# Performance work log

Measured on AMD Instinct MI355X. Metric: run time of the kernel, lower is better.

Reference implementation:

```python
import jax, jax.numpy as jnp
import numpy as np

D_MODEL = 1024
NHEAD = 16
D_HEAD = D_MODEL // NHEAD


def setup_inputs() -> dict:
    key = jax.random.key(0)
    ks = jax.random.split(key, 9)
    B, S = 2, 2048
    scale = 1.0 / np.sqrt(D_MODEL)
    x = jax.random.normal(ks[0], (B, S, D_MODEL), dtype=jnp.float32)
    Wq = jax.random.normal(ks[1], (D_MODEL, D_MODEL), dtype=jnp.float32) * scale
    Wk = jax.random.normal(ks[2], (D_MODEL, D_MODEL), dtype=jnp.float32) * scale
    Wv = jax.random.normal(ks[3], (D_MODEL, D_MODEL), dtype=jnp.float32) * scale
    Wo = jax.random.normal(ks[4], (D_MODEL, D_MODEL), dtype=jnp.float32) * scale
    bq = jax.random.normal(ks[5], (D_MODEL,), dtype=jnp.float32) * 0.01
    bk = jax.random.normal(ks[6], (D_MODEL,), dtype=jnp.float32) * 0.01
    bv = jax.random.normal(ks[7], (D_MODEL,), dtype=jnp.float32) * 0.01
    bo = jax.random.normal(ks[8], (D_MODEL,), dtype=jnp.float32) * 0.01
    return {"x": x, "Wq": Wq, "bq": bq, "Wk": Wk, "bk": bk,
            "Wv": Wv, "bv": bv, "Wo": Wo, "bo": bo}


def reference(x, Wq, bq, Wk, bk, Wv, bv, Wo, bo):
    B, S, D = x.shape
    H, Dh = NHEAD, D_HEAD
    # projections; weights stored as (in, out) so y = x @ W + b
    def split_heads(t):  # [B,S,D] -> [B,H,S,Dh]
        return t.reshape(B, S, H, Dh).transpose(0, 2, 1, 3)
    q = split_heads(x @ Wq + bq)
    k = split_heads(x @ Wk + bk)
    v = split_heads(x @ Wv + bv)
    scale = 1.0 / jnp.sqrt(jnp.asarray(Dh, dtype=x.dtype))
    attn = jnp.einsum("bhqd,bhkd->bhqk", q, k) * scale  # [B,H,S,S]
    attn = jax.nn.softmax(attn, axis=-1)
    out = jnp.einsum("bhqk,bhkd->bhqd", attn, v)  # [B,H,S,Dh]
    out = out.transpose(0, 2, 1, 3).reshape(B, S, D)
    return out @ Wo + bo
```

## Files before the change

kernel.cpp:

```cpp
#include <hip/hip_runtime.h>
#include <hip/hip_bf16.h>
#include <stdint.h>
#include <stddef.h>

typedef __bf16 b16;
typedef __bf16 b16x4 __attribute__((ext_vector_type(4)));
typedef __bf16 b16x8 __attribute__((ext_vector_type(8)));
typedef float  f32x4 __attribute__((ext_vector_type(4)));

#define LOG2E 1.4426950408889634f
#define QSCALE (0.125f * LOG2E)

#if __has_builtin(__builtin_amdgcn_exp2f)
#define EXP2F(x) __builtin_amdgcn_exp2f(x)
#else
#define EXP2F(x) exp2f(x)
#endif

typedef __attribute__((address_space(1))) void gvoid;
typedef __attribute__((address_space(3))) void svoid;

__device__ __forceinline__ void async_cp16(void* lds, const void* g) {
    __builtin_amdgcn_global_load_lds((gvoid*)(void*)g, (svoid*)lds, 16, 0, 0);
}

#define SW(r) ((((r) & 7)) ^ (((r) >> 1) & 4))

__global__ __launch_bounds__(256) void k_cvt_x(const float* __restrict__ x,
                                               b16* __restrict__ xb) {
    int i = (blockIdx.x * 256 + threadIdx.x) * 4;
    float4 v = *(const float4*)(x + i);
    b16x4 o = { (b16)v.x, (b16)v.y, (b16)v.z, (b16)v.w };
    *(b16x4*)(xb + i) = o;
}

__global__ __launch_bounds__(256) void k_transpose(const float* __restrict__ Wq,
                                                   const float* __restrict__ Wk,
                                                   const float* __restrict__ Wv,
                                                   const float* __restrict__ Wo,
                                                   b16* __restrict__ WtQKV,
                                                   b16* __restrict__ Wot) {
    __shared__ float t[32][33];
    const int z = blockIdx.z;
    const float* W = (z == 0) ? Wq : (z == 1) ? Wk : (z == 2) ? Wv : Wo;
    const int k0 = blockIdx.x * 32, n0 = blockIdx.y * 32;
    const int tr = threadIdx.x >> 3, tc4 = (threadIdx.x & 7) * 4;
    float4 v = *(const float4*)(W + (size_t)(k0 + tr) * 1024 + n0 + tc4);
    t[tr][tc4 + 0] = v.x; t[tr][tc4 + 1] = v.y;
    t[tr][tc4 + 2] = v.z; t[tr][tc4 + 3] = v.w;
    __syncthreads();
    b16* dst = (z < 3) ? (WtQKV + ((size_t)z << 20)) : Wot;
    b16x4 o = { (b16)t[tc4 + 0][tr], (b16)t[tc4 + 1][tr],
                (b16)t[tc4 + 2][tr], (b16)t[tc4 + 3][tr] };
    *(b16x4*)(dst + (size_t)(n0 + tr) * 1024 + k0 + tc4) = o;
}

__device__ __forceinline__ void gemm128_core(const b16* __restrict__ Ab,
                                             const b16* __restrict__ Bb,
                                             b16* As, b16* Bs, int tid,
                                             f32x4 acc[4][4]) {
    const int lane = tid & 63, wave = tid >> 6;
    const int wm = wave & 1, wn = wave >> 1;
    const int quad = lane >> 4, lc = lane & 15;
    const int ci0 = tid, ci1 = tid + 256;
    for (int k0 = 0; k0 < 1024; k0 += 32) {
        __syncthreads();
        async_cp16(As + ci0 * 8, Ab + (ci0 >> 2) * 1024 + k0 + (ci0 & 3) * 8);
        async_cp16(As + ci1 * 8, Ab + (ci1 >> 2) * 1024 + k0 + (ci1 & 3) * 8);
        async_cp16(Bs + ci0 * 8, Bb + (ci0 >> 2) * 1024 + k0 + (ci0 & 3) * 8);
        async_cp16(Bs + ci1 * 8, Bb + (ci1 >> 2) * 1024 + k0 + (ci1 & 3) * 8);
        __syncthreads();
        b16x8 af[4], bfr[4];
#pragma unroll
        for (int mt = 0; mt < 4; ++mt)
            af[mt] = *(const b16x8*)(As + (wm * 64 + mt * 16 + lc) * 32 + quad * 8);
#pragma unroll
        for (int nt = 0; nt < 4; ++nt)
            bfr[nt] = *(const b16x8*)(Bs + (wn * 64 + nt * 16 + lc) * 32 + quad * 8);
#pragma unroll
        for (int mt = 0; mt < 4; ++mt)
#pragma unroll
            for (int nt = 0; nt < 4; ++nt)
                acc[mt][nt] = __builtin_amdgcn_mfma_f32_16x16x32_bf16(
                    af[mt], bfr[nt], acc[mt][nt], 0, 0, 0);
    }
}

__global__ __launch_bounds__(256, 2) void k_gemm_qkv(
    const b16* __restrict__ A, const b16* __restrict__ Bt,
    const float* __restrict__ bq, const float* __restrict__ bk,
    const float* __restrict__ bv,
    b16* __restrict__ Qg, b16* __restrict__ Kg, b16* __restrict__ Vtg) {
    __shared__ __align__(16) b16 As[128 * 32];
    __shared__ __align__(16) b16 Bs[128 * 32];
    const int bm = blockIdx.x, bn = blockIdx.y;
    const int tid = threadIdx.x;
    const int lane = tid & 63, wave = tid >> 6;
    const int wm = wave & 1, wn = wave >> 1;
    const int quad = lane >> 4, lc = lane & 15;

    f32x4 acc[4][4] = {};
    gemm128_core(A + (size_t)(bm * 128) * 1024, Bt + (size_t)(bn * 128) * 1024,
                 As, Bs, tid, acc);

    const int mat = bn >> 3;
    const float* bp = (mat == 0) ? bq : (mat == 1) ? bk : bv;
#pragma unroll
    for (int nt = 0; nt < 4; ++nt) {
        const int n = bn * 128 + wn * 64 + nt * 16 + lc;
        const int cm = n & 1023;
        const int h = cm >> 6, dh = cm & 63;
        const float bval = bp[cm];
#pragma unroll
        for (int mt = 0; mt < 4; ++mt) {
            const int m0 = bm * 128 + wm * 64 + mt * 16 + quad * 4;
            const int b = m0 >> 11;
            const int bh = b * 16 + h;
            const int s0 = m0 & 2047;
            if (mat == 2) {
                b16x4 o;
#pragma unroll
                for (int r = 0; r < 4; ++r) o[r] = (b16)(acc[mt][nt][r] + bval);
                *(b16x4*)(Vtg + (size_t)(bh * 64 + dh) * 2048 + s0) = o;
            } else if (mat == 0) {
#pragma unroll
                for (int r = 0; r < 4; ++r)
                    Qg[(size_t)(bh * 2048 + s0 + r) * 64 + dh] =
                        (b16)((acc[mt][nt][r] + bval) * QSCALE);
            } else {
#pragma unroll
                for (int r = 0; r < 4; ++r)
                    Kg[(size_t)(bh * 2048 + s0 + r) * 64 + dh] =
                        (b16)(acc[mt][nt][r] + bval);
            }
        }
    }
}

__device__ __forceinline__ void flash_stage(b16* Kd, b16* Vd,
                                            const b16* __restrict__ Kbh,
                                            const b16* __restrict__ Vbh,
                                            int kt, int tid) {
#pragma unroll
    for (int i = 0; i < 2; ++i) {
        const int ci = tid + i * 256;
        const int r = ci >> 3, cs = ci & 7;
        const int gc = cs ^ SW(r);
        async_cp16(Kd + ci * 8, Kbh + (size_t)(kt * 64 + r) * 64 + gc * 8);
        async_cp16(Vd + ci * 8, Vbh + (size_t)r * 2048 + kt * 64 + gc * 8);
    }
}

__global__ __launch_bounds__(256, 4) void k_flash(
    const b16* __restrict__ Qg, const b16* __restrict__ Kg,
    const b16* __restrict__ Vtg,
    float* __restrict__ Opart, float* __restrict__ lpart,
    b16* __restrict__ AO, int ktiles, int direct, int np) {
    __shared__ __align__(16) b16 Ks[2 * 64 * 64];
    __shared__ __align__(16) b16 Vs[2 * 64 * 64];
    __shared__ float Lred[4][32];

    const int bid = blockIdx.x;
    const int gstride = np << 5;
    const int qb = bid / gstride;
    const int rem = bid - qb * gstride;
    const int bh = rem / np;
    const int part = rem - bh * np;

    const int tid = threadIdx.x, lane = tid & 63, wave = tid >> 6;
    const int quad = lane >> 4, lc = lane & 15;

    const b16* Kbh = Kg + (size_t)bh * 2048 * 64;
    const b16* Vbh = Vtg + (size_t)bh * 64 * 2048;
    const int kt0 = part * ktiles, ktE = kt0 + ktiles;

    flash_stage(Ks, Vs, Kbh, Vbh, kt0, tid);

    const b16* Qbase = Qg + ((size_t)bh * 2048 + qb * 128 + wave * 32) * 64;
    b16x8 qf[2][2];
#pragma unroll
    for (int qt = 0; qt < 2; ++qt)
#pragma unroll
        for (int ch = 0; ch < 2; ++ch)
            qf[qt][ch] = *(const b16x8*)(Qbase + (qt * 16 + lc) * 64 + ch * 32 + quad * 8);

    f32x4 oacc[2][4] = {};
    float lsum[2] = {0.f, 0.f};

    for (int kt = kt0; kt < ktE; ++kt) {
        const int cur = (kt - kt0) & 1;
        const b16* Kc = Ks + cur * 4096;
        const b16* Vc = Vs + cur * 4096;

        if (kt + 1 < ktE) {
            flash_stage(Ks + (cur ^ 1) * 4096, Vs + (cur ^ 1) * 4096,
                        Kbh, Vbh, kt + 1, tid);
            asm volatile("s_waitcnt vmcnt(4)" ::: "memory");
        } else {
            asm volatile("s_waitcnt vmcnt(0)" ::: "memory");
        }
        __builtin_amdgcn_s_barrier();
        __builtin_amdgcn_sched_barrier(0);

#pragma unroll
        for (int ks = 0; ks < 2; ++ks) {
            b16x8 pf[2];
#pragma unroll
            for (int t = 0; t < 2; ++t) {
                const int krow = ks * 32 + (lc >> 2) * 8 + t * 4 + (lc & 3);
                b16x8 kf[2];
#pragma unroll
                for (int ch = 0; ch < 2; ++ch) {
                    const int slot = (ch * 4 + quad) ^ SW(krow);
                    kf[ch] = *(const b16x8*)(Kc + krow * 64 + slot * 8);
                }
#pragma unroll
                for (int qt = 0; qt < 2; ++qt) {
                    f32x4 s = {};
                    __builtin_amdgcn_s_setprio(1);
                    s = __builtin_amdgcn_mfma_f32_16x16x32_bf16(kf[0], qf[qt][0], s, 0, 0, 0);
                    s = __builtin_amdgcn_mfma_f32_16x16x32_bf16(kf[1], qf[qt][1], s, 0, 0, 0);
                    __builtin_amdgcn_s_setprio(0);
                    float e0 = EXP2F(s[0]), e1 = EXP2F(s[1]);
                    float e2 = EXP2F(s[2]), e3 = EXP2F(s[3]);
                    lsum[qt] += (e0 + e1) + (e2 + e3);
                    pf[qt][t * 4 + 0] = (b16)e0;
                    pf[qt][t * 4 + 1] = (b16)e1;
                    pf[qt][t * 4 + 2] = (b16)e2;
                    pf[qt][t * 4 + 3] = (b16)e3;
                }
            }
            b16x8 vf[4];
#pragma unroll
            for (int dt = 0; dt < 4; ++dt) {
                const int row = dt * 16 + lc;
                const int slot = (ks * 4 + quad) ^ SW(row);
                vf[dt] = *(const b16x8*)(Vc + row * 64 + slot * 8);
            }
            __builtin_amdgcn_s_setprio(1);
#pragma unroll
            for (int qt = 0; qt < 2; ++qt)
#pragma unroll
                for (int dt = 0; dt < 4; ++dt)
                    oacc[qt][dt] = __builtin_amdgcn_mfma_f32_16x16x32_bf16(
                        pf[qt], vf[dt], oacc[qt][dt], 0, 0, 0);
            __builtin_amdgcn_s_setprio(0);
        }

        __builtin_amdgcn_sched_barrier(0);
        __builtin_amdgcn_s_barrier();
    }

#pragma unroll
    for (int qt = 0; qt < 2; ++qt) {
        lsum[qt] += __shfl_xor(lsum[qt], 16, 64);
        lsum[qt] += __shfl_xor(lsum[qt], 32, 64);
    }

    if (!direct) {
        float* Op = Opart + ((size_t)(part * 32 + bh) * 2048 + qb * 128 + wave * 32) * 64;
#pragma unroll
        for (int qt = 0; qt < 2; ++qt)
#pragma unroll
            for (int dt = 0; dt < 4; ++dt)
#pragma unroll
                for (int r = 0; r < 4; ++r)
                    Op[(qt * 16 + quad * 4 + r) * 64 + dt * 16 + lc] = oacc[qt][dt][r];
        if (quad == 0) {
            float* lp = lpart + (size_t)(part * 32 + bh) * 2048 + qb * 128 + wave * 32;
#pragma unroll
            for (int qt = 0; qt < 2; ++qt) lp[qt * 16 + lc] = lsum[qt];
        }
    } else {
        if (quad == 0) {
#pragma unroll
            for (int qt = 0; qt < 2; ++qt) Lred[wave][qt * 16 + lc] = lsum[qt];
        }
        const int b = bh >> 4, h = bh & 15;
#pragma unroll
        for (int qt = 0; qt < 2; ++qt)
#pragma unroll
            for (int r = 0; r < 4; ++r) {
                const float inv = 1.0f / Lred[wave][qt * 16 + quad * 4 + r];
                const int s = qb * 128 + wave * 32 + qt * 16 + quad * 4 + r;
#pragma unroll
                for (int dt = 0; dt < 4; ++dt)
                    AO[(size_t)(b * 2048 + s) * 1024 + h * 64 + dt * 16 + lc] =
                        (b16)(oacc[qt][dt][r] * inv);
            }
    }
}

__global__ __launch_bounds__(256) void k_merge(const float* __restrict__ Opart,
                                               const float* __restrict__ lpart,
                                               b16* __restrict__ AO, int np) {
    const int bh = blockIdx.y;
    const int q = blockIdx.x * 16 + (threadIdx.x >> 4);
    const int d4 = (threadIdx.x & 15) * 4;
    const size_t qi = (size_t)bh * 2048 + q;
    f32x4 o = *(const f32x4*)(Opart + qi * 64 + d4);
    float l = lpart[qi];
    if (np == 2) {
        o += *(const f32x4*)(Opart + (qi + (size_t)32 * 2048) * 64 + d4);
        l += lpart[qi + (size_t)32 * 2048];
    }
    const float inv = 1.0f / l;
    const int b = bh >> 4, h = bh & 15;
    b16x4 ob = { (b16)(o[0] * inv), (b16)(o[1] * inv),
                 (b16)(o[2] * inv), (b16)(o[3] * inv) };
    *(b16x4*)(AO + (size_t)(b * 2048 + q) * 1024 + h * 64 + d4) = ob;
}

__global__ __launch_bounds__(256, 2) void k_gemm_out(
    const b16* __restrict__ A, const b16* __restrict__ Bt,
    const float* __restrict__ bo, float* __restrict__ out) {
    __shared__ __align__(16) b16 As[128 * 32];
    __shared__ __align__(16) b16 Bs[128 * 32];
    const int bm = blockIdx.x, bn = blockIdx.y;
    const int tid = threadIdx.x;
    const int lane = tid & 63, wave = tid >> 6;
    const int wm = wave & 1, wn = wave >> 1;
    const int quad = lane >> 4, lc = lane & 15;

    f32x4 acc[4][4] = {};
    gemm128_core(A + (size_t)(bm * 128) * 1024, Bt + (size_t)(bn * 128) * 1024,
                 As, Bs, tid, acc);

#pragma unroll
    for (int nt = 0; nt < 4; ++nt) {
        const int n = bn * 128 + wn * 64 + nt * 16 + lc;
        const float bval = bo[n];
#pragma unroll
        for (int mt = 0; mt < 4; ++mt) {
            const int m0 = bm * 128 + wm * 64 + mt * 16 + quad * 4;
#pragma unroll
            for (int r = 0; r < 4; ++r)
                out[(size_t)(m0 + r) * 1024 + n] = acc[mt][nt][r] + bval;
        }
    }
}

extern "C" void kernel_launch(void* const* d_in, const int* in_sizes, int n_in,
                              void* d_out, int out_size, void* d_ws, size_t ws_size,
                              hipStream_t stream) {
    const float* x  = (const float*)d_in[0];
    const float* Wq = (const float*)d_in[1];
    const float* bq = (const float*)d_in[2];
    const float* Wk = (const float*)d_in[3];
    const float* bk = (const float*)d_in[4];
    const float* Wv = (const float*)d_in[5];
    const float* bv = (const float*)d_in[6];
    const float* Wo = (const float*)d_in[7];
    const float* bo = (const float*)d_in[8];
    float* out = (float*)d_out;

    char* ws = (char*)d_ws;
    const size_t MB = 1024 * 1024;
    b16* Xb  = (b16*)(ws);
    b16* AO  = (b16*)(ws);
    b16* WtQ = (b16*)(ws + 8 * MB);
    b16* Wot = (b16*)(ws + 14 * MB);
    b16* Qg  = (b16*)(ws + 16 * MB);
    b16* Kg  = (b16*)(ws + 24 * MB);
    b16* Vtg = (b16*)(ws + 32 * MB);

    const size_t need2 = 40 * MB + 2 * (16 * MB) + 2 * 256 * 1024;
    const int np = (ws_size >= need2) ? 2 : 1;
    float* Opart = (float*)(ws + 40 * MB);
    float* lpart = (float*)(ws + 40 * MB + (size_t)np * 16 * MB);
    const int direct = (np == 1);

    k_cvt_x<<<4096, 256, 0, stream>>>(x, Xb);
    k_transpose<<<dim3(32, 32, 4), 256, 0, stream>>>(Wq, Wk, Wv, Wo, WtQ, Wot);
    k_gemm_qkv<<<dim3(32, 24), 256, 0, stream>>>(Xb, WtQ, bq, bk, bv, Qg, Kg, Vtg);
    k_flash<<<dim3(16 * 32 * np), 256, 0, stream>>>(Qg, Kg, Vtg, Opart, lpart, AO,
                                                    32 / np, direct, np);
    if (!direct)
        k_merge<<<dim3(128, 32), 256, 0, stream>>>(Opart, lpart, AO, np);
    k_gemm_out<<<dim3(32, 8), 256, 0, stream>>>(AO, Wot, bo, out);
}
```

Measured before the change: 197.1 us.

## Double-buffer GEMM loads, drop flash key split, fuse prep kernels

```diff
diff --git a/kernel.cpp b/kernel.cpp
--- a/kernel.cpp
+++ b/kernel.cpp
@@ -26,22 +26,29 @@
 
 #define SW(r) ((((r) & 7)) ^ (((r) >> 1) & 4))
 
-__global__ __launch_bounds__(256) void k_cvt_x(const float* __restrict__ x,
-                                               b16* __restrict__ xb) {
-    int i = (blockIdx.x * 256 + threadIdx.x) * 4;
-    float4 v = *(const float4*)(x + i);
-    b16x4 o = { (b16)v.x, (b16)v.y, (b16)v.z, (b16)v.w };
-    *(b16x4*)(xb + i) = o;
-}
-
-__global__ __launch_bounds__(256) void k_transpose(const float* __restrict__ Wq,
-                                                   const float* __restrict__ Wk,
-                                                   const float* __restrict__ Wv,
-                                                   const float* __restrict__ Wo,
-                                                   b16* __restrict__ WtQKV,
-                                                   b16* __restrict__ Wot) {
+__global__ __launch_bounds__(256) void k_prep(const float* __restrict__ x,
+                                              const float* __restrict__ Wq,
+                                              const float* __restrict__ Wk,
+                                              const float* __restrict__ Wv,
+                                              const float* __restrict__ Wo,
+                                              b16* __restrict__ Xb,
+                                              b16* __restrict__ WtQKV,
+                                              b16* __restrict__ Wot) {
+    const int z = blockIdx.z;
+    if (z == 4) {
+        const int blk = blockIdx.y * 32 + blockIdx.x;
+        const float* src = x + (size_t)blk * 4096;
+        b16* dst = Xb + (size_t)blk * 4096;
+#pragma unroll
+        for (int c = 0; c < 4; ++c) {
+            const int i = c * 1024 + threadIdx.x * 4;
+            float4 v = *(const float4*)(src + i);
+            b16x4 o = { (b16)v.x, (b16)v.y, (b16)v.z, (b16)v.w };
+            *(b16x4*)(dst + i) = o;
+        }
+        return;
+    }
     __shared__ float t[32][33];
-    const int z = blockIdx.z;
     const float* W = (z == 0) ? Wq : (z == 1) ? Wk : (z == 2) ? Wv : Wo;
     const int k0 = blockIdx.x * 32, n0 = blockIdx.y * 32;
     const int tr = threadIdx.x >> 3, tc4 = (threadIdx.x & 7) * 4;
@@ -55,35 +62,66 @@
     *(b16x4*)(dst + (size_t)(n0 + tr) * 1024 + k0 + tc4) = o;
 }
 
-__device__ __forceinline__ void gemm128_core(const b16* __restrict__ Ab,
-                                             const b16* __restrict__ Bb,
+__device__ __forceinline__ void gemm128_core(const b16* __restrict__ Ag,
+                                             const b16* __restrict__ Bg,
                                              b16* As, b16* Bs, int tid,
                                              f32x4 acc[4][4]) {
     const int lane = tid & 63, wave = tid >> 6;
     const int wm = wave & 1, wn = wave >> 1;
     const int quad = lane >> 4, lc = lane & 15;
     const int ci0 = tid, ci1 = tid + 256;
-    for (int k0 = 0; k0 < 1024; k0 += 32) {
-        __syncthreads();
-        async_cp16(As + ci0 * 8, Ab + (ci0 >> 2) * 1024 + k0 + (ci0 & 3) * 8);
-        async_cp16(As + ci1 * 8, Ab + (ci1 >> 2) * 1024 + k0 + (ci1 & 3) * 8);
-        async_cp16(Bs + ci0 * 8, Bb + (ci0 >> 2) * 1024 + k0 + (ci0 & 3) * 8);
-        async_cp16(Bs + ci1 * 8, Bb + (ci1 >> 2) * 1024 + k0 + (ci1 & 3) * 8);
-        __syncthreads();
+    const b16* a0 = Ag + (ci0 >> 2) * 1024 + (ci0 & 3) * 8;
+    const b16* a1 = Ag + (ci1 >> 2) * 1024 + (ci1 & 3) * 8;
+    const b16* b0 = Bg + (ci0 >> 2) * 1024 + (ci0 & 3) * 8;
+    const b16* b1 = Bg + (ci1 >> 2) * 1024 + (ci1 & 3) * 8;
+
+#define GSTAGE(BUF, K0) do {                                   \
+        async_cp16(As + (BUF) * 4096 + ci0 * 8, a0 + (K0));    \
+        async_cp16(As + (BUF) * 4096 + ci1 * 8, a1 + (K0));    \
+        async_cp16(Bs + (BUF) * 4096 + ci0 * 8, b0 + (K0));    \
+        async_cp16(Bs + (BUF) * 4096 + ci1 * 8, b1 + (K0));    \
+    } while (0)
+
+    auto gcompute = [&](int buf) {
+        const b16* Al = As + buf * 4096;
+        const b16* Bl = Bs + buf * 4096;
         b16x8 af[4], bfr[4];
 #pragma unroll
         for (int mt = 0; mt < 4; ++mt)
-            af[mt] = *(const b16x8*)(As + (wm * 64 + mt * 16 + lc) * 32 + quad * 8);
+            af[mt] = *(const b16x8*)(Al + (wm * 64 + mt * 16 + lc) * 32 + quad * 8);
 #pragma unroll
         for (int nt = 0; nt < 4; ++nt)
-            bfr[nt] = *(const b16x8*)(Bs + (wn * 64 + nt * 16 + lc) * 32 + quad * 8);
+            bfr[nt] = *(const b16x8*)(Bl + (wn * 64 + nt * 16 + lc) * 32 + quad * 8);
 #pragma unroll
         for (int mt = 0; mt < 4; ++mt)
 #pragma unroll
             for (int nt = 0; nt < 4; ++nt)
                 acc[mt][nt] = __builtin_amdgcn_mfma_f32_16x16x32_bf16(
                     af[mt], bfr[nt], acc[mt][nt], 0, 0, 0);
-    }
+    };
+
+    GSTAGE(0, 0);
+    for (int k0 = 0; k0 < 1024; k0 += 64) {
+        GSTAGE(1, k0 + 32);
+        asm volatile("s_waitcnt vmcnt(4)" ::: "memory");
+        __builtin_amdgcn_s_barrier();
+        __builtin_amdgcn_sched_barrier(0);
+        gcompute(0);
+        __builtin_amdgcn_sched_barrier(0);
+        __builtin_amdgcn_s_barrier();
+        if (k0 + 64 < 1024) {
+            GSTAGE(0, k0 + 64);
+            asm volatile("s_waitcnt vmcnt(4)" ::: "memory");
+        } else {
+            asm volatile("s_waitcnt vmcnt(0)" ::: "memory");
+        }
+        __builtin_amdgcn_s_barrier();
+        __builtin_amdgcn_sched_barrier(0);
+        gcompute(1);
+        __builtin_amdgcn_sched_barrier(0);
+        __builtin_amdgcn_s_barrier();
+    }
+#undef GSTAGE
 }
 
 __global__ __launch_bounds__(256, 2) void k_gemm_qkv(
@@ -91,8 +129,8 @@
     const float* __restrict__ bq, const float* __restrict__ bk,
     const float* __restrict__ bv,
     b16* __restrict__ Qg, b16* __restrict__ Kg, b16* __restrict__ Vtg) {
-    __shared__ __align__(16) b16 As[128 * 32];
-    __shared__ __align__(16) b16 Bs[128 * 32];
+    __shared__ __align__(16) b16 As[2 * 128 * 32];
+    __shared__ __align__(16) b16 Bs[2 * 128 * 32];
     const int bm = blockIdx.x, bn = blockIdx.y;
     const int tid = threadIdx.x;
     const int lane = tid & 63, wave = tid >> 6;
@@ -137,185 +175,128 @@
     }
 }
 
-__device__ __forceinline__ void flash_stage(b16* Kd, b16* Vd,
-                                            const b16* __restrict__ Kbh,
-                                            const b16* __restrict__ Vbh,
-                                            int kt, int tid) {
-#pragma unroll
-    for (int i = 0; i < 2; ++i) {
-        const int ci = tid + i * 256;
-        const int r = ci >> 3, cs = ci & 7;
-        const int gc = cs ^ SW(r);
-        async_cp16(Kd + ci * 8, Kbh + (size_t)(kt * 64 + r) * 64 + gc * 8);
-        async_cp16(Vd + ci * 8, Vbh + (size_t)r * 2048 + kt * 64 + gc * 8);
-    }
-}
-
 __global__ __launch_bounds__(256, 4) void k_flash(
     const b16* __restrict__ Qg, const b16* __restrict__ Kg,
-    const b16* __restrict__ Vtg,
-    float* __restrict__ Opart, float* __restrict__ lpart,
-    b16* __restrict__ AO, int ktiles, int direct, int np) {
+    const b16* __restrict__ Vtg, b16* __restrict__ AO) {
     __shared__ __align__(16) b16 Ks[2 * 64 * 64];
     __shared__ __align__(16) b16 Vs[2 * 64 * 64];
-    __shared__ float Lred[4][32];
+    __shared__ float Lred[4][16];
 
     const int bid = blockIdx.x;
-    const int gstride = np << 5;
-    const int qb = bid / gstride;
-    const int rem = bid - qb * gstride;
-    const int bh = rem / np;
-    const int part = rem - bh * np;
+    const int qb = bid >> 5;
+    const int bh = bid & 31;
 
     const int tid = threadIdx.x, lane = tid & 63, wave = tid >> 6;
     const int quad = lane >> 4, lc = lane & 15;
 
     const b16* Kbh = Kg + (size_t)bh * 2048 * 64;
     const b16* Vbh = Vtg + (size_t)bh * 64 * 2048;
-    const int kt0 = part * ktiles, ktE = kt0 + ktiles;
-
-    flash_stage(Ks, Vs, Kbh, Vbh, kt0, tid);
-
-    const b16* Qbase = Qg + ((size_t)bh * 2048 + qb * 128 + wave * 32) * 64;
-    b16x8 qf[2][2];
-#pragma unroll
-    for (int qt = 0; qt < 2; ++qt)
-#pragma unroll
-        for (int ch = 0; ch < 2; ++ch)
-            qf[qt][ch] = *(const b16x8*)(Qbase + (qt * 16 + lc) * 64 + ch * 32 + quad * 8);
-
-    f32x4 oacc[2][4] = {};
-    float lsum[2] = {0.f, 0.f};
-
-    for (int kt = kt0; kt < ktE; ++kt) {
-        const int cur = (kt - kt0) & 1;
-        const b16* Kc = Ks + cur * 4096;
-        const b16* Vc = Vs + cur * 4096;
-
-        if (kt + 1 < ktE) {
-            flash_stage(Ks + (cur ^ 1) * 4096, Vs + (cur ^ 1) * 4096,
-                        Kbh, Vbh, kt + 1, tid);
+
+    const int ci0 = tid, ci1 = tid + 256;
+    const int r0 = ci0 >> 3, gc0 = (ci0 & 7) ^ SW(r0);
+    const int r1 = ci1 >> 3, gc1 = (ci1 & 7) ^ SW(r1);
+    const b16* pK0 = Kbh + r0 * 64 + gc0 * 8;
+    const b16* pK1 = Kbh + r1 * 64 + gc1 * 8;
+    const b16* pV0 = Vbh + (size_t)r0 * 2048 + gc0 * 8;
+    const b16* pV1 = Vbh + (size_t)r1 * 2048 + gc1 * 8;
+
+#define FSTAGE(BUF) do {                                   \
+        async_cp16(Ks + (BUF) * 4096 + ci0 * 8, pK0);      \
+        async_cp16(Ks + (BUF) * 4096 + ci1 * 8, pK1);      \
+        async_cp16(Vs + (BUF) * 4096 + ci0 * 8, pV0);      \
+        async_cp16(Vs + (BUF) * 4096 + ci1 * 8, pV1);      \
+        pK0 += 4096; pK1 += 4096; pV0 += 64; pV1 += 64;    \
+    } while (0)
+
+    FSTAGE(0);
+
+    const b16* Qbase = Qg + ((size_t)bh * 2048 + qb * 64 + wave * 16) * 64;
+    b16x8 qf0 = *(const b16x8*)(Qbase + lc * 64 + quad * 8);
+    b16x8 qf1 = *(const b16x8*)(Qbase + lc * 64 + 32 + quad * 8);
+
+    f32x4 oacc[4] = {};
+    float lsum = 0.f;
+
+    auto flash_tile = [&](const b16* Kc, const b16* Vc) {
+#pragma unroll
+        for (int ks = 0; ks < 2; ++ks) {
+            b16x8 pf;
+#pragma unroll
+            for (int t = 0; t < 2; ++t) {
+                const int krow = ks * 32 + (lc >> 2) * 8 + t * 4 + (lc & 3);
+                b16x8 kf0 = *(const b16x8*)(Kc + krow * 64 + ((0 * 4 + quad) ^ SW(krow)) * 8);
+                b16x8 kf1 = *(const b16x8*)(Kc + krow * 64 + ((1 * 4 + quad) ^ SW(krow)) * 8);
+                f32x4 s = {};
+                __builtin_amdgcn_s_setprio(1);
+                s = __builtin_amdgcn_mfma_f32_16x16x32_bf16(kf0, qf0, s, 0, 0, 0);
+                s = __builtin_amdgcn_mfma_f32_16x16x32_bf16(kf1, qf1, s, 0, 0, 0);
+                __builtin_amdgcn_s_setprio(0);
+                float e0 = EXP2F(s[0]), e1 = EXP2F(s[1]);
+                float e2 = EXP2F(s[2]), e3 = EXP2F(s[3]);
+                lsum += (e0 + e1) + (e2 + e3);
+                pf[t * 4 + 0] = (b16)e0;
+                pf[t * 4 + 1] = (b16)e1;
+                pf[t * 4 + 2] = (b16)e2;
+                pf[t * 4 + 3] = (b16)e3;
+            }
+            b16x8 vf[4];
+#pragma unroll
+            for (int dt = 0; dt < 4; ++dt) {
+                const int row = dt * 16 + lc;
+                vf[dt] = *(const b16x8*)(Vc + row * 64 + ((ks * 4 + quad) ^ SW(row)) * 8);
+            }
+            __builtin_amdgcn_s_setprio(1);
+#pragma unroll
+            for (int dt = 0; dt < 4; ++dt)
+                oacc[dt] = __builtin_amdgcn_mfma_f32_16x16x32_bf16(
+                    pf, vf[dt], oacc[dt], 0, 0, 0);
+            __builtin_amdgcn_s_setprio(0);
+        }
+    };
+
+    for (int kt = 0; kt < 32; kt += 2) {
+        FSTAGE(1);
+        asm volatile("s_waitcnt vmcnt(4)" ::: "memory");
+        __builtin_amdgcn_s_barrier();
+        __builtin_amdgcn_sched_barrier(0);
+        flash_tile(Ks, Vs);
+        __builtin_amdgcn_sched_barrier(0);
+        __builtin_amdgcn_s_barrier();
+        if (kt + 2 < 32) {
+            FSTAGE(0);
             asm volatile("s_waitcnt vmcnt(4)" ::: "memory");
         } else {
             asm volatile("s_waitcnt vmcnt(0)" ::: "memory");
         }
         __builtin_amdgcn_s_barrier();
         __builtin_amdgcn_sched_barrier(0);
-
-#pragma unroll
-        for (int ks = 0; ks < 2; ++ks) {
-            b16x8 pf[2];
-#pragma unroll
-            for (int t = 0; t < 2; ++t) {
-                const int krow = ks * 32 + (lc >> 2) * 8 + t * 4 + (lc & 3);
-                b16x8 kf[2];
-#pragma unroll
-                for (int ch = 0; ch < 2; ++ch) {
-                    const int slot = (ch * 4 + quad) ^ SW(krow);
-                    kf[ch] = *(const b16x8*)(Kc + krow * 64 + slot * 8);
-                }
-#pragma unroll
-                for (int qt = 0; qt < 2; ++qt) {
-                    f32x4 s = {};
-                    __builtin_amdgcn_s_setprio(1);
-                    s = __builtin_amdgcn_mfma_f32_16x16x32_bf16(kf[0], qf[qt][0], s, 0, 0, 0);
-                    s = __builtin_amdgcn_mfma_f32_16x16x32_bf16(kf[1], qf[qt][1], s, 0, 0, 0);
-                    __builtin_amdgcn_s_setprio(0);
-                    float e0 = EXP2F(s[0]), e1 = EXP2F(s[1]);
-                    float e2 = EXP2F(s[2]), e3 = EXP2F(s[3]);
-                    lsum[qt] += (e0 + e1) + (e2 + e3);
-                    pf[qt][t * 4 + 0] = (b16)e0;
-                    pf[qt][t * 4 + 1] = (b16)e1;
-                    pf[qt][t * 4 + 2] = (b16)e2;
-                    pf[qt][t * 4 + 3] = (b16)e3;
-                }
-            }
-            b16x8 vf[4];
-#pragma unroll
-            for (int dt = 0; dt < 4; ++dt) {
-                const int row = dt * 16 + lc;
-                const int slot = (ks * 4 + quad) ^ SW(row);
-                vf[dt] = *(const b16x8*)(Vc + row * 64 + slot * 8);
-            }
-            __builtin_amdgcn_s_setprio(1);
-#pragma unroll
-            for (int qt = 0; qt < 2; ++qt)
-#pragma unroll
-                for (int dt = 0; dt < 4; ++dt)
-                    oacc[qt][dt] = __builtin_amdgcn_mfma_f32_16x16x32_bf16(
-                        pf[qt], vf[dt], oacc[qt][dt], 0, 0, 0);
-            __builtin_amdgcn_s_setprio(0);
-        }
-
-        __builtin_amdgcn_sched_barrier(0);
-        __builtin_amdgcn_s_barrier();
-    }
-
-#pragma unroll
-    for (int qt = 0; qt < 2; ++qt) {
-        lsum[qt] += __shfl_xor(lsum[qt], 16, 64);
-        lsum[qt] += __shfl_xor(lsum[qt], 32, 64);
-    }
-
-    if (!direct) {
-        float* Op = Opart + ((size_t)(part * 32 + bh) * 2048 + qb * 128 + wave * 32) * 64;
-#pragma unroll
-        for (int qt = 0; qt < 2; ++qt)
-#pragma unroll
-            for (int dt = 0; dt < 4; ++dt)
-#pragma unroll
-                for (int r = 0; r < 4; ++r)
-                    Op[(qt * 16 + quad * 4 + r) * 64 + dt * 16 + lc] = oacc[qt][dt][r];
-        if (quad == 0) {
-            float* lp = lpart + (size_t)(part * 32 + bh) * 2048 + qb * 128 + wave * 32;
-#pragma unroll
-            for (int qt = 0; qt < 2; ++qt) lp[qt * 16 + lc] = lsum[qt];
-        }
-    } else {
-        if (quad == 0) {
-#pragma unroll
-            for (int qt = 0; qt < 2; ++qt) Lred[wave][qt * 16 + lc] = lsum[qt];
-        }
-        const int b = bh >> 4, h = bh & 15;
-#pragma unroll
-        for (int qt = 0; qt < 2; ++qt)
-#pragma unroll
-            for (int r = 0; r < 4; ++r) {
-                const float inv = 1.0f / Lred[wave][qt * 16 + quad * 4 + r];
-                const int s = qb * 128 + wave * 32 + qt * 16 + quad * 4 + r;
-#pragma unroll
-                for (int dt = 0; dt < 4; ++dt)
-                    AO[(size_t)(b * 2048 + s) * 1024 + h * 64 + dt * 16 + lc] =
-                        (b16)(oacc[qt][dt][r] * inv);
-            }
-    }
-}
-
-__global__ __launch_bounds__(256) void k_merge(const float* __restrict__ Opart,
-                                               const float* __restrict__ lpart,
-                                               b16* __restrict__ AO, int np) {
-    const int bh = blockIdx.y;
-    const int q = blockIdx.x * 16 + (threadIdx.x >> 4);
-    const int d4 = (threadIdx.x & 15) * 4;
-    const size_t qi = (size_t)bh * 2048 + q;
-    f32x4 o = *(const f32x4*)(Opart + qi * 64 + d4);
-    float l = lpart[qi];
-    if (np == 2) {
-        o += *(const f32x4*)(Opart + (qi + (size_t)32 * 2048) * 64 + d4);
-        l += lpart[qi + (size_t)32 * 2048];
-    }
-    const float inv = 1.0f / l;
+        flash_tile(Ks + 4096, Vs + 4096);
+        __builtin_amdgcn_sched_barrier(0);
+        __builtin_amdgcn_s_barrier();
+    }
+#undef FSTAGE
+
+    lsum += __shfl_xor(lsum, 16, 64);
+    lsum += __shfl_xor(lsum, 32, 64);
+
+    if (quad == 0) Lred[wave][lc] = lsum;
     const int b = bh >> 4, h = bh & 15;
-    b16x4 ob = { (b16)(o[0] * inv), (b16)(o[1] * inv),
-                 (b16)(o[2] * inv), (b16)(o[3] * inv) };
-    *(b16x4*)(AO + (size_t)(b * 2048 + q) * 1024 + h * 64 + d4) = ob;
+#pragma unroll
+    for (int r = 0; r < 4; ++r) {
+        const float inv = 1.0f / Lred[wave][quad * 4 + r];
+        const int s = qb * 64 + wave * 16 + quad * 4 + r;
+#pragma unroll
+        for (int dt = 0; dt < 4; ++dt)
+            AO[(size_t)(b * 2048 + s) * 1024 + h * 64 + dt * 16 + lc] =
+                (b16)(oacc[dt][r] * inv);
+    }
 }
 
 __global__ __launch_bounds__(256, 2) void k_gemm_out(
     const b16* __restrict__ A, const b16* __restrict__ Bt,
     const float* __restrict__ bo, float* __restrict__ out) {
-    __shared__ __align__(16) b16 As[128 * 32];
-    __shared__ __align__(16) b16 Bs[128 * 32];
+    __shared__ __align__(16) b16 As[2 * 128 * 32];
+    __shared__ __align__(16) b16 Bs[2 * 128 * 32];
     const int bm = blockIdx.x, bn = blockIdx.y;
     const int tid = threadIdx.x;
     const int lane = tid & 63, wave = tid >> 6;
@@ -364,18 +345,8 @@
     b16* Kg  = (b16*)(ws + 24 * MB);
     b16* Vtg = (b16*)(ws + 32 * MB);
 
-    const size_t need2 = 40 * MB + 2 * (16 * MB) + 2 * 256 * 1024;
-    const int np = (ws_size >= need2) ? 2 : 1;
-    float* Opart = (float*)(ws + 40 * MB);
-    float* lpart = (float*)(ws + 40 * MB + (size_t)np * 16 * MB);
-    const int direct = (np == 1);
-
-    k_cvt_x<<<4096, 256, 0, stream>>>(x, Xb);
-    k_transpose<<<dim3(32, 32, 4), 256, 0, stream>>>(Wq, Wk, Wv, Wo, WtQ, Wot);
+    k_prep<<<dim3(32, 32, 5), 256, 0, stream>>>(x, Wq, Wk, Wv, Wo, Xb, WtQ, Wot);
     k_gemm_qkv<<<dim3(32, 24), 256, 0, stream>>>(Xb, WtQ, bq, bk, bv, Qg, Kg, Vtg);
-    k_flash<<<dim3(16 * 32 * np), 256, 0, stream>>>(Qg, Kg, Vtg, Opart, lpart, AO,
-                                                    32 / np, direct, np);
-    if (!direct)
-        k_merge<<<dim3(128, 32), 256, 0, stream>>>(Opart, lpart, AO, np);
+    k_flash<<<dim3(1024), 256, 0, stream>>>(Qg, Kg, Vtg, AO);
     k_gemm_out<<<dim3(32, 8), 256, 0, stream>>>(AO, Wot, bo, out);
 }
```

Measured after the change: 188.7 us. 4.2% less time.
